# Optimization experiments

Hardware: AMD Instinct MI355X
Metric: run time of the kernel (lower is better)

The kernel has to match this reference:

```python
import jax, jax.numpy as jnp
import numpy as np

D_IN = 1024
D_OUT = 1024


def setup_inputs() -> dict:
    key = jax.random.key(0)
    k_x, k_q, k_k, k_v = jax.random.split(key, 4)
    x = jax.random.normal(k_x, (8, 2048, D_IN), dtype=jnp.float32)
    s = 1.0 / np.sqrt(D_IN)
    W_query = jax.random.uniform(k_q, (D_IN, D_OUT), jnp.float32, -s, s)
    W_key = jax.random.uniform(k_k, (D_IN, D_OUT), jnp.float32, -s, s)
    W_value = jax.random.uniform(k_v, (D_IN, D_OUT), jnp.float32, -s, s)
    return {"x": x, "W_query": W_query, "W_key": W_key, "W_value": W_value}


def reference(x, W_query, W_key, W_value):
    # x: [B, N, d_in]; weights stored as [d_in, d_out] (already transposed vs torch Linear)
    B, N, _ = x.shape
    q = x @ W_query          # [B, N, d_out]
    k = x @ W_key
    v = x @ W_value
    scores = jnp.einsum('bnd,bmd->bnm', q, k)  # [B, N, N]
    causal = jnp.tril(jnp.ones((N, N), dtype=bool))
    scores = jnp.where(causal, scores, -jnp.inf)
    weights = jax.nn.softmax(scores / np.sqrt(D_OUT), axis=-1)
    # dropout p=0.0 -> identity
    return jnp.einsum('bnm,bmd->bnd', weights, v)
```

## Files before the change

### kernel.cpp

```cpp
#include <hip/hip_runtime.h>
#include <hip/hip_bf16.h>

typedef unsigned short u16;
typedef unsigned int u32;
typedef __bf16 bf16x8 __attribute__((ext_vector_type(8)));
typedef float f32x4 __attribute__((ext_vector_type(4)));
typedef unsigned int u32x4 __attribute__((ext_vector_type(4)));

#define BATCH 8
#define SEQ   2048
#define DIM   1024
#define M_TOT (BATCH * SEQ)
#define N_QKV (3 * DIM)

#define OFF_QKV  ((size_t)0)
#define OFF_VT   ((size_t)100663296)
#define OFF_C    ((size_t)134217728)
#define OFF_XB   OFF_C
#define OFF_WT   (OFF_C + (size_t)33554432)
#define OFF_S    OFF_C

__device__ __forceinline__ u16 f32_to_bf16(float f) {
    u32 u = __builtin_bit_cast(u32, f);
    u = (u + 0x7fffu + ((u >> 16) & 1u)) >> 16;
    return (u16)u;
}

__device__ __forceinline__ float bf16_to_f32(u16 h) {
    u32 u = ((u32)h) << 16;
    return __builtin_bit_cast(float, u);
}

__device__ __forceinline__ bf16x8 lds_load8(const u16* p) {
    return __builtin_bit_cast(bf16x8, *(const u32x4*)p);
}

#define UNIT 8192

__device__ __forceinline__ void stage_unit(const u16* g, size_t lda, int k0,
                                           u16* lds, int tid) {
    int wv = tid >> 6;
#pragma unroll
    for (int iss = 0; iss < 2; ++iss) {
        int s = iss * 512 + tid;
        int row = s >> 2;
        int kg = (s & 3) ^ (row & 3);
        const u16* gp = g + (size_t)row * lda + (k0 + (kg << 3));
        u16* lp = lds + (size_t)(iss * 512 + wv * 64) * 8;
        __builtin_amdgcn_global_load_lds((const __attribute__((address_space(1))) void*)gp,
                                         (__attribute__((address_space(3))) void*)lp,
                                         16, 0, 0);
    }
}

template <int MH>
__device__ __forceinline__ void mfma_phase(const u16* uA, const u16* uB, int lane,
                                           int wm, int wn, f32x4 acc[8][4]) {
    int lrow = lane & 15;
    int off = (((lane >> 4) ^ (lane & 3)) << 3);
    bf16x8 a[4], b[4];
#pragma unroll
    for (int i = 0; i < 4; ++i) {
        a[i] = lds_load8(&uA[(wm * 128 + (MH * 4 + i) * 16 + lrow) * 32 + off]);
        b[i] = lds_load8(&uB[(wn * 64 + i * 16 + lrow) * 32 + off]);
    }
    __builtin_amdgcn_s_setprio(1);
#pragma unroll
    for (int i = 0; i < 4; ++i)
#pragma unroll
        for (int j = 0; j < 4; ++j)
            acc[MH * 4 + i][j] =
                __builtin_amdgcn_mfma_f32_16x16x32_bf16(a[i], b[j], acc[MH * 4 + i][j], 0, 0, 0);
    __builtin_amdgcn_s_setprio(0);
}

__device__ __forceinline__ void gemm_block_256(const u16* __restrict__ A, size_t lda,
                                               const u16* __restrict__ B, size_t ldb,
                                               int KT, u16* lds, int tid,
                                               f32x4 acc[8][4]) {
    int lane = tid & 63;
    int wv = tid >> 6;
    int wm = wv >> 2, wn = wv & 3;
    stage_unit(A, lda, 0,  lds + 0 * UNIT, tid);
    stage_unit(B, ldb, 0,  lds + 4 * UNIT, tid);
    stage_unit(A, lda, 32, lds + 1 * UNIT, tid);
    stage_unit(B, ldb, 32, lds + 5 * UNIT, tid);
    for (int t = 0; t < KT; ++t) {
        int p = t & 1, pn = p ^ 1;
        int kb = (t + 1) << 6;
        bool pf = (t + 1 < KT);
        asm volatile("s_waitcnt vmcnt(4)" ::: "memory");
        __builtin_amdgcn_s_barrier();
        if (pf) stage_unit(A, lda, kb, lds + (size_t)(pn * 2) * UNIT, tid);
        mfma_phase<0>(lds + (size_t)(p * 2) * UNIT, lds + (size_t)(4 + p * 2) * UNIT,
                      lane, wm, wn, acc);
        __builtin_amdgcn_s_barrier();
        if (pf) stage_unit(B, ldb, kb, lds + (size_t)(4 + pn * 2) * UNIT, tid);
        mfma_phase<1>(lds + (size_t)(p * 2) * UNIT, lds + (size_t)(4 + p * 2) * UNIT,
                      lane, wm, wn, acc);
        __builtin_amdgcn_s_barrier();
        if (pf) { asm volatile("s_waitcnt vmcnt(4)" ::: "memory"); }
        else    { asm volatile("s_waitcnt vmcnt(0)" ::: "memory"); }
        __builtin_amdgcn_s_barrier();
        if (pf) stage_unit(A, lda, kb + 32, lds + (size_t)(pn * 2 + 1) * UNIT, tid);
        mfma_phase<0>(lds + (size_t)(p * 2 + 1) * UNIT, lds + (size_t)(4 + p * 2 + 1) * UNIT,
                      lane, wm, wn, acc);
        __builtin_amdgcn_s_barrier();
        if (pf) stage_unit(B, ldb, kb + 32, lds + (size_t)(4 + pn * 2 + 1) * UNIT, tid);
        mfma_phase<1>(lds + (size_t)(p * 2 + 1) * UNIT, lds + (size_t)(4 + p * 2 + 1) * UNIT,
                      lane, wm, wn, acc);
    }
}

__global__ __launch_bounds__(256) void cast_x_kernel(const float* __restrict__ x,
                                                     u16* __restrict__ xb) {
    size_t g = (size_t)blockIdx.x * 256 + threadIdx.x;
    f32x4 v = ((const f32x4*)x)[g];
    u16 o[4] = {f32_to_bf16(v.x), f32_to_bf16(v.y), f32_to_bf16(v.z), f32_to_bf16(v.w)};
    *(unsigned long long*)(xb + g * 4) = *(const unsigned long long*)o;
}

__global__ __launch_bounds__(256) void transpose_w_kernel(const float* __restrict__ wq,
                                                          const float* __restrict__ wk,
                                                          const float* __restrict__ wv,
                                                          u16* __restrict__ wt) {
    __shared__ __align__(16) u16 tile[64][80];
    const float* w = blockIdx.z == 0 ? wq : (blockIdx.z == 1 ? wk : wv);
    int k0 = blockIdx.x * 64, n0 = blockIdx.y * 64;
    for (int g = threadIdx.x; g < 1024; g += 256) {
        int r = g >> 4, c = (g & 15) << 2;
        f32x4 v = *(const f32x4*)(w + (size_t)(k0 + r) * 1024 + n0 + c);
        tile[r][c + 0] = f32_to_bf16(v.x);
        tile[r][c + 1] = f32_to_bf16(v.y);
        tile[r][c + 2] = f32_to_bf16(v.z);
        tile[r][c + 3] = f32_to_bf16(v.w);
    }
    __syncthreads();
    u16* out = wt + (size_t)blockIdx.z * 1024 * 1024;
    for (int g = threadIdx.x; g < 512; g += 256) {
        int nr = g >> 3, kc = (g & 7) << 3;
        __align__(16) u16 tmp[8];
#pragma unroll
        for (int i = 0; i < 8; ++i) tmp[i] = tile[kc + i][nr];
        *(u32x4*)(out + (size_t)(n0 + nr) * 1024 + k0 + kc) = *(const u32x4*)tmp;
    }
}

__global__ __launch_bounds__(512, 2) void gemm_qkv_kernel(const u16* __restrict__ xb,
                                                          const u16* __restrict__ wt,
                                                          u16* __restrict__ qkv) {
    __shared__ __align__(16) u16 lds[8 * UNIT];
    int wg = blockIdx.x;
    int qx = gridDim.x >> 3;
    int swz = (wg & 7) * qx + (wg >> 3);
    int mt = swz / 12, nt = swz - mt * 12;
    const u16* A = xb + (size_t)mt * 256 * 1024;
    const u16* B = wt + (size_t)nt * 256 * 1024;
    int tid = threadIdx.x;
    f32x4 acc[8][4] = {};
    gemm_block_256(A, 1024, B, 1024, 16, lds, tid, acc);
    int lane = tid & 63, wv = tid >> 6;
    int wm = wv >> 2, wn = wv & 3;
    int r0 = (lane >> 4) << 2, c0 = lane & 15;
    size_t mbase = (size_t)mt * 256 + wm * 128;
    int nbase = nt * 256 + wn * 64;
#pragma unroll
    for (int i = 0; i < 8; ++i)
#pragma unroll
        for (int j = 0; j < 4; ++j) {
            int col = nbase + j * 16 + c0;
            float scale = (col < 1024) ? 0.03125f : 1.0f;
#pragma unroll
            for (int r = 0; r < 4; ++r) {
                size_t row = mbase + i * 16 + r0 + r;
                qkv[row * (size_t)N_QKV + col] = f32_to_bf16(acc[i][j][r] * scale);
            }
        }
}

__global__ __launch_bounds__(256) void transpose_v_kernel(const u16* __restrict__ qkv,
                                                          u16* __restrict__ vt) {
    __shared__ __align__(16) u16 tile[64][80];
    int m0 = blockIdx.x * 64, d0 = blockIdx.y * 64, b = blockIdx.z;
    const u16* src = qkv + (size_t)b * SEQ * N_QKV + 2048;
    for (int g = threadIdx.x; g < 512; g += 256) {
        int r = g >> 3, c = (g & 7) << 3;
        *(u32x4*)&tile[r][c] = *(const u32x4*)(src + (size_t)(m0 + r) * N_QKV + d0 + c);
    }
    __syncthreads();
    u16* dst = vt + (size_t)b * DIM * SEQ;
    for (int g = threadIdx.x; g < 512; g += 256) {
        int dr = g >> 3, mc = (g & 7) << 3;
        __align__(16) u16 tmp[8];
#pragma unroll
        for (int i = 0; i < 8; ++i) tmp[i] = tile[mc + i][dr];
        *(u32x4*)(dst + (size_t)(d0 + dr) * SEQ + m0 + mc) = *(const u32x4*)tmp;
    }
}

__global__ __launch_bounds__(512, 2) void gemm_scores_kernel(const u16* __restrict__ qkv,
                                                             u16* __restrict__ S) {
    __shared__ __align__(16) u16 lds[8 * UNIT];
    int t = blockIdx.x;
    int b = blockIdx.y;
    int ntile = 0;
#pragma unroll
    for (int it = 1; it < 8; ++it)
        if ((it * (it + 1)) / 2 <= t) ntile = it;
    int mtile = t - (ntile * (ntile + 1)) / 2;
    const u16* A = qkv + (size_t)b * SEQ * N_QKV + (size_t)ntile * 256 * N_QKV;
    const u16* B = qkv + (size_t)b * SEQ * N_QKV + (size_t)mtile * 256 * N_QKV + 1024;
    int tid = threadIdx.x;
    f32x4 acc[8][4] = {};
    gemm_block_256(A, N_QKV, B, N_QKV, 16, lds, tid, acc);
    u16* out = S + (size_t)b * SEQ * SEQ + (size_t)ntile * 256 * SEQ + (size_t)mtile * 256;
    int lane = tid & 63, wv = tid >> 6;
    int wm = wv >> 2, wn = wv & 3;
    int r0 = (lane >> 4) << 2, c0 = lane & 15;
#pragma unroll
    for (int i = 0; i < 8; ++i)
#pragma unroll
        for (int j = 0; j < 4; ++j) {
            int col = wn * 64 + j * 16 + c0;
#pragma unroll
            for (int r = 0; r < 4; ++r) {
                int row = wm * 128 + i * 16 + r0 + r;
                out[(size_t)row * SEQ + col] = f32_to_bf16(acc[i][j][r]);
            }
        }
}

__global__ __launch_bounds__(256) void softmax_kernel(u16* __restrict__ SP) {
    int gr = blockIdx.x;
    int n = gr & 2047;
    u16* s = SP + (size_t)gr * SEQ;
    __shared__ float red[4];
    int t = threadIdx.x;
    int base = t << 3;
    int len = n + 1;
    float v[8];
    float lmax = -3.0e38f;
    if (base < len) {
        u32x4 raw = *(const u32x4*)(s + base);
        const u16* h = (const u16*)&raw;
#pragma unroll
        for (int i = 0; i < 8; ++i) {
            v[i] = (base + i < len) ? bf16_to_f32(h[i]) : -3.0e38f;
            lmax = fmaxf(lmax, v[i]);
        }
    } else {
#pragma unroll
        for (int i = 0; i < 8; ++i) v[i] = -3.0e38f;
    }
#pragma unroll
    for (int off = 32; off; off >>= 1) lmax = fmaxf(lmax, __shfl_xor(lmax, off, 64));
    if ((t & 63) == 0) red[t >> 6] = lmax;
    __syncthreads();
    float gmax = fmaxf(fmaxf(red[0], red[1]), fmaxf(red[2], red[3]));
    __syncthreads();
    float lsum = 0.f;
#pragma unroll
    for (int i = 0; i < 8; ++i) {
        float e = __expf(v[i] - gmax);
        v[i] = e;
        lsum += e;
    }
#pragma unroll
    for (int off = 32; off; off >>= 1) lsum += __shfl_xor(lsum, off, 64);
    if ((t & 63) == 0) red[t >> 6] = lsum;
    __syncthreads();
    float inv = 1.0f / (red[0] + red[1] + red[2] + red[3]);
    __align__(16) u16 o[8];
#pragma unroll
    for (int i = 0; i < 8; ++i) o[i] = f32_to_bf16(v[i] * inv);
    *(u32x4*)(s + base) = *(const u32x4*)o;
}

__global__ __launch_bounds__(512, 2) void gemm_out_kernel(const u16* __restrict__ P,
                                                          const u16* __restrict__ vt,
                                                          float* __restrict__ O) {
    __shared__ __align__(16) u16 lds[8 * UNIT];
    int dt = blockIdx.x, b = blockIdx.z;
    int ntile = (SEQ / 256 - 1) - blockIdx.y;
    const u16* A = P + (size_t)b * SEQ * SEQ + (size_t)ntile * 256 * SEQ;
    const u16* B = vt + (size_t)b * DIM * SEQ + (size_t)dt * 256 * SEQ;
    int tid = threadIdx.x;
    f32x4 acc[8][4] = {};
    int KT = (ntile + 1) * 4;
    gemm_block_256(A, SEQ, B, SEQ, KT, lds, tid, acc);
    float* out = O + (size_t)b * SEQ * DIM + (size_t)ntile * 256 * DIM + (size_t)dt * 256;
    int lane = tid & 63, wv = tid >> 6;
    int wm = wv >> 2, wn = wv & 3;
    int r0 = (lane >> 4) << 2, c0 = lane & 15;
#pragma unroll
    for (int i = 0; i < 8; ++i)
#pragma unroll
        for (int j = 0; j < 4; ++j) {
            int col = wn * 64 + j * 16 + c0;
#pragma unroll
            for (int r = 0; r < 4; ++r) {
                int row = wm * 128 + i * 16 + r0 + r;
                out[(size_t)row * DIM + col] = acc[i][j][r];
            }
        }
}

extern "C" void kernel_launch(void* const* d_in, const int* in_sizes, int n_in,
                              void* d_out, int out_size, void* d_ws, size_t ws_size,
                              hipStream_t stream) {
    const float* x = (const float*)d_in[0];
    const float* wq = (const float*)d_in[1];
    const float* wk = (const float*)d_in[2];
    const float* wv = (const float*)d_in[3];
    char* ws = (char*)d_ws;
    u16* qkv = (u16*)(ws + OFF_QKV);
    u16* vt = (u16*)(ws + OFF_VT);
    u16* xb = (u16*)(ws + OFF_XB);
    u16* wt = (u16*)(ws + OFF_WT);
    u16* S = (u16*)(ws + OFF_S);
    float* O = (float*)d_out;

    cast_x_kernel<<<M_TOT * DIM / 4 / 256, 256, 0, stream>>>(x, xb);
    transpose_w_kernel<<<dim3(16, 16, 3), 256, 0, stream>>>(wq, wk, wv, wt);
    gemm_qkv_kernel<<<(M_TOT / 256) * (N_QKV / 256), 512, 0, stream>>>(xb, wt, qkv);
    transpose_v_kernel<<<dim3(SEQ / 64, DIM / 64, BATCH), 256, 0, stream>>>(qkv, vt);
    gemm_scores_kernel<<<dim3(36, BATCH), 512, 0, stream>>>(qkv, S);
    softmax_kernel<<<BATCH * SEQ, 256, 0, stream>>>(S);
    gemm_out_kernel<<<dim3(DIM / 256, SEQ / 256, BATCH), 512, 0, stream>>>(S, vt, O);
}
```

Before: 401.9 us.

## Deepen GEMM prefetch to a five-slot ring and remap blocks across XCDs

Result: faster. 393.3 us (-2.2%).

```diff
diff --git a/kernel.cpp b/kernel.cpp
--- a/kernel.cpp
+++ b/kernel.cpp
@@ -35,35 +35,39 @@
     return __builtin_bit_cast(bf16x8, *(const u32x4*)p);
 }
 
-#define UNIT 8192
-
-__device__ __forceinline__ void stage_unit(const u16* g, size_t lda, int k0,
-                                           u16* lds, int tid) {
+#define U4 2048
+#define NSLOT 20
+
+__device__ __forceinline__ void stage_pair(const u16* g, size_t lda, int k0,
+                                           int qbase, u16* lpair, int tid) {
     int wv = tid >> 6;
-#pragma unroll
-    for (int iss = 0; iss < 2; ++iss) {
-        int s = iss * 512 + tid;
-        int row = s >> 2;
-        int kg = (s & 3) ^ (row & 3);
-        const u16* gp = g + (size_t)row * lda + (k0 + (kg << 3));
-        u16* lp = lds + (size_t)(iss * 512 + wv * 64) * 8;
-        __builtin_amdgcn_global_load_lds((const __attribute__((address_space(1))) void*)gp,
-                                         (__attribute__((address_space(3))) void*)lp,
-                                         16, 0, 0);
+    int lane = tid & 63;
+    int u = wv >> 2;
+    int su = ((wv & 3) << 6) + lane;
+    int row = su >> 2, sc = su & 3;
+    int c = sc ^ ((row >> 1) & 3);
+    const u16* gp = g + (size_t)((qbase + u) * 64 + row) * lda + k0 + (c << 3);
+    u16* lp = lpair + u * U4 + ((wv & 3) << 9);
+    __builtin_amdgcn_global_load_lds((const __attribute__((address_space(1))) void*)gp,
+                                     (__attribute__((address_space(3))) void*)lp,
+                                     16, 0, 0);
+}
+
+template <bool LOADB>
+__device__ __forceinline__ void frags_read(const u16* uA, const u16* uB, int lane,
+                                           bf16x8 a[4], bf16x8 b[4]) {
+    int lrow = lane & 15, kgl = lane >> 4;
+    int sl = (kgl ^ ((lrow >> 1) & 3)) << 3;
+#pragma unroll
+    for (int i = 0; i < 4; ++i) {
+        a[i] = lds_load8(&uA[(i * 16 + lrow) * 32 + sl]);
+        if (LOADB) b[i] = lds_load8(&uB[(i * 16 + lrow) * 32 + sl]);
     }
 }
 
 template <int MH>
-__device__ __forceinline__ void mfma_phase(const u16* uA, const u16* uB, int lane,
-                                           int wm, int wn, f32x4 acc[8][4]) {
-    int lrow = lane & 15;
-    int off = (((lane >> 4) ^ (lane & 3)) << 3);
-    bf16x8 a[4], b[4];
-#pragma unroll
-    for (int i = 0; i < 4; ++i) {
-        a[i] = lds_load8(&uA[(wm * 128 + (MH * 4 + i) * 16 + lrow) * 32 + off]);
-        b[i] = lds_load8(&uB[(wn * 64 + i * 16 + lrow) * 32 + off]);
-    }
+__device__ __forceinline__ void mfma16(const bf16x8 a[4], const bf16x8 b[4],
+                                       f32x4 acc[8][4]) {
     __builtin_amdgcn_s_setprio(1);
 #pragma unroll
     for (int i = 0; i < 4; ++i)
@@ -76,39 +80,55 @@
 
 __device__ __forceinline__ void gemm_block_256(const u16* __restrict__ A, size_t lda,
                                                const u16* __restrict__ B, size_t ldb,
-                                               int KT, u16* lds, int tid,
+                                               int KT, u16* ldsA, u16* ldsB, int tid,
                                                f32x4 acc[8][4]) {
     int lane = tid & 63;
     int wv = tid >> 6;
     int wm = wv >> 2, wn = wv & 3;
-    stage_unit(A, lda, 0,  lds + 0 * UNIT, tid);
-    stage_unit(B, ldb, 0,  lds + 4 * UNIT, tid);
-    stage_unit(A, lda, 32, lds + 1 * UNIT, tid);
-    stage_unit(B, ldb, 32, lds + 5 * UNIT, tid);
+#pragma unroll
+    for (int pt = 0; pt < 4; ++pt) {
+        stage_pair(A, lda, pt << 5, 0, ldsA + (pt * 4 + 0) * U4, tid);
+        stage_pair(A, lda, pt << 5, 2, ldsA + (pt * 4 + 2) * U4, tid);
+        stage_pair(B, ldb, pt << 5, 0, ldsB + (pt * 4 + 0) * U4, tid);
+        stage_pair(B, ldb, pt << 5, 2, ldsB + (pt * 4 + 2) * U4, tid);
+    }
+    asm volatile("s_waitcnt vmcnt(12)" ::: "memory");
+    __builtin_amdgcn_s_barrier();
+    int rt = 0, rs = 4;
     for (int t = 0; t < KT; ++t) {
-        int p = t & 1, pn = p ^ 1;
-        int kb = (t + 1) << 6;
-        bool pf = (t + 1 < KT);
-        asm volatile("s_waitcnt vmcnt(4)" ::: "memory");
+        const u16* uA0 = ldsA + (rt * 4 + wm * 2) * U4;
+        const u16* uA1 = uA0 + U4;
+        const u16* uB  = ldsB + (rt * 4 + wn) * U4;
+        bool pf = (t + 4 < KT);
+        int k4 = (t + 4) << 5;
+        bf16x8 a[4], b[4];
+        frags_read<true>(uA0, uB, lane, a, b);
+        if (pf) {
+            stage_pair(A, lda, k4, 0, ldsA + (rs * 4 + 0) * U4, tid);
+            stage_pair(A, lda, k4, 2, ldsA + (rs * 4 + 2) * U4, tid);
+        }
         __builtin_amdgcn_s_barrier();
-        if (pf) stage_unit(A, lda, kb, lds + (size_t)(pn * 2) * UNIT, tid);
-        mfma_phase<0>(lds + (size_t)(p * 2) * UNIT, lds + (size_t)(4 + p * 2) * UNIT,
-                      lane, wm, wn, acc);
+        asm volatile("s_waitcnt lgkmcnt(0)" ::: "memory");
+        mfma16<0>(a, b, acc);
         __builtin_amdgcn_s_barrier();
-        if (pf) stage_unit(B, ldb, kb, lds + (size_t)(4 + pn * 2) * UNIT, tid);
-        mfma_phase<1>(lds + (size_t)(p * 2) * UNIT, lds + (size_t)(4 + p * 2) * UNIT,
-                      lane, wm, wn, acc);
+        frags_read<false>(uA1, uB, lane, a, b);
+        if (pf) {
+            stage_pair(B, ldb, k4, 0, ldsB + (rs * 4 + 0) * U4, tid);
+            stage_pair(B, ldb, k4, 2, ldsB + (rs * 4 + 2) * U4, tid);
+            asm volatile("s_waitcnt vmcnt(12)" ::: "memory");
+        } else if (t + 3 < KT) {
+            asm volatile("s_waitcnt vmcnt(8)" ::: "memory");
+        } else if (t + 2 < KT) {
+            asm volatile("s_waitcnt vmcnt(4)" ::: "memory");
+        } else if (t + 1 < KT) {
+            asm volatile("s_waitcnt vmcnt(0)" ::: "memory");
+        }
         __builtin_amdgcn_s_barrier();
-        if (pf) { asm volatile("s_waitcnt vmcnt(4)" ::: "memory"); }
-        else    { asm volatile("s_waitcnt vmcnt(0)" ::: "memory"); }
+        asm volatile("s_waitcnt lgkmcnt(0)" ::: "memory");
+        mfma16<1>(a, b, acc);
         __builtin_amdgcn_s_barrier();
-        if (pf) stage_unit(A, lda, kb + 32, lds + (size_t)(pn * 2 + 1) * UNIT, tid);
-        mfma_phase<0>(lds + (size_t)(p * 2 + 1) * UNIT, lds + (size_t)(4 + p * 2 + 1) * UNIT,
-                      lane, wm, wn, acc);
-        __builtin_amdgcn_s_barrier();
-        if (pf) stage_unit(B, ldb, kb + 32, lds + (size_t)(4 + pn * 2 + 1) * UNIT, tid);
-        mfma_phase<1>(lds + (size_t)(p * 2 + 1) * UNIT, lds + (size_t)(4 + p * 2 + 1) * UNIT,
-                      lane, wm, wn, acc);
+        rt = (rt == 4) ? 0 : rt + 1;
+        rs = (rs == 4) ? 0 : rs + 1;
     }
 }
 
@@ -149,16 +169,21 @@
 __global__ __launch_bounds__(512, 2) void gemm_qkv_kernel(const u16* __restrict__ xb,
                                                           const u16* __restrict__ wt,
                                                           u16* __restrict__ qkv) {
-    __shared__ __align__(16) u16 lds[8 * UNIT];
+    __shared__ __align__(16) u16 lds[2 * NSLOT * U4];
+    u16* ldsA = lds;
+    u16* ldsB = lds + NSLOT * U4;
     int wg = blockIdx.x;
-    int qx = gridDim.x >> 3;
-    int swz = (wg & 7) * qx + (wg >> 3);
-    int mt = swz / 12, nt = swz - mt * 12;
+    int xcd = wg & 7;
+    int r = wg >> 3;
+    int ng = r >> 5;
+    int j = r & 31;
+    int mt = xcd * 8 + (j & 7);
+    int nt = ng * 4 + (j >> 3);
     const u16* A = xb + (size_t)mt * 256 * 1024;
     const u16* B = wt + (size_t)nt * 256 * 1024;
     int tid = threadIdx.x;
     f32x4 acc[8][4] = {};
-    gemm_block_256(A, 1024, B, 1024, 16, lds, tid, acc);
+    gemm_block_256(A, 1024, B, 1024, 32, ldsA, ldsB, tid, acc);
     int lane = tid & 63, wv = tid >> 6;
     int wm = wv >> 2, wn = wv & 3;
     int r0 = (lane >> 4) << 2, c0 = lane & 15;
@@ -167,13 +192,13 @@
 #pragma unroll
     for (int i = 0; i < 8; ++i)
 #pragma unroll
-        for (int j = 0; j < 4; ++j) {
-            int col = nbase + j * 16 + c0;
+        for (int jj = 0; jj < 4; ++jj) {
+            int col = nbase + jj * 16 + c0;
             float scale = (col < 1024) ? 0.03125f : 1.0f;
 #pragma unroll
-            for (int r = 0; r < 4; ++r) {
-                size_t row = mbase + i * 16 + r0 + r;
-                qkv[row * (size_t)N_QKV + col] = f32_to_bf16(acc[i][j][r] * scale);
+            for (int rr = 0; rr < 4; ++rr) {
+                size_t row = mbase + i * 16 + r0 + rr;
+                qkv[row * (size_t)N_QKV + col] = f32_to_bf16(acc[i][jj][rr] * scale);
             }
         }
 }
@@ -200,9 +225,12 @@
 
 __global__ __launch_bounds__(512, 2) void gemm_scores_kernel(const u16* __restrict__ qkv,
                                                              u16* __restrict__ S) {
-    __shared__ __align__(16) u16 lds[8 * UNIT];
-    int t = blockIdx.x;
-    int b = blockIdx.y;
+    __shared__ __align__(16) u16 lds[2 * NSLOT * U4];
+    u16* ldsA = lds;
+    u16* ldsB = lds + NSLOT * U4;
+    int wg = blockIdx.x;
+    int b = wg & 7;
+    int t = wg >> 3;
     int ntile = 0;
 #pragma unroll
     for (int it = 1; it < 8; ++it)
@@ -212,7 +240,7 @@
     const u16* B = qkv + (size_t)b * SEQ * N_QKV + (size_t)mtile * 256 * N_QKV + 1024;
     int tid = threadIdx.x;
     f32x4 acc[8][4] = {};
-    gemm_block_256(A, N_QKV, B, N_QKV, 16, lds, tid, acc);
+    gemm_block_256(A, N_QKV, B, N_QKV, 32, ldsA, ldsB, tid, acc);
     u16* out = S + (size_t)b * SEQ * SEQ + (size_t)ntile * 256 * SEQ + (size_t)mtile * 256;
     int lane = tid & 63, wv = tid >> 6;
     int wm = wv >> 2, wn = wv & 3;
@@ -220,12 +248,12 @@
 #pragma unroll
     for (int i = 0; i < 8; ++i)
 #pragma unroll
-        for (int j = 0; j < 4; ++j) {
-            int col = wn * 64 + j * 16 + c0;
-#pragma unroll
-            for (int r = 0; r < 4; ++r) {
-                int row = wm * 128 + i * 16 + r0 + r;
-                out[(size_t)row * SEQ + col] = f32_to_bf16(acc[i][j][r]);
+        for (int jj = 0; jj < 4; ++jj) {
+            int col = wn * 64 + jj * 16 + c0;
+#pragma unroll
+            for (int rr = 0; rr < 4; ++rr) {
+                int row = wm * 128 + i * 16 + r0 + rr;
+                out[(size_t)row * SEQ + col] = f32_to_bf16(acc[i][jj][rr]);
             }
         }
 }
@@ -279,15 +307,20 @@
 __global__ __launch_bounds__(512, 2) void gemm_out_kernel(const u16* __restrict__ P,
                                                           const u16* __restrict__ vt,
                                                           float* __restrict__ O) {
-    __shared__ __align__(16) u16 lds[8 * UNIT];
-    int dt = blockIdx.x, b = blockIdx.z;
-    int ntile = (SEQ / 256 - 1) - blockIdx.y;
+    __shared__ __align__(16) u16 lds[2 * NSLOT * U4];
+    u16* ldsA = lds;
+    u16* ldsB = lds + NSLOT * U4;
+    int wg = blockIdx.x;
+    int b = wg & 7;
+    int r = wg >> 3;
+    int dt = r & 3;
+    int ntile = r >> 2;
     const u16* A = P + (size_t)b * SEQ * SEQ + (size_t)ntile * 256 * SEQ;
     const u16* B = vt + (size_t)b * DIM * SEQ + (size_t)dt * 256 * SEQ;
     int tid = threadIdx.x;
     f32x4 acc[8][4] = {};
-    int KT = (ntile + 1) * 4;
-    gemm_block_256(A, SEQ, B, SEQ, KT, lds, tid, acc);
+    int KT = (ntile + 1) * 8;
+    gemm_block_256(A, SEQ, B, SEQ, KT, ldsA, ldsB, tid, acc);
     float* out = O + (size_t)b * SEQ * DIM + (size_t)ntile * 256 * DIM + (size_t)dt * 256;
     int lane = tid & 63, wv = tid >> 6;
     int wm = wv >> 2, wn = wv & 3;
@@ -295,12 +328,12 @@
 #pragma unroll
     for (int i = 0; i < 8; ++i)
 #pragma unroll
-        for (int j = 0; j < 4; ++j) {
-            int col = wn * 64 + j * 16 + c0;
-#pragma unroll
-            for (int r = 0; r < 4; ++r) {
-                int row = wm * 128 + i * 16 + r0 + r;
-                out[(size_t)row * DIM + col] = acc[i][j][r];
+        for (int jj = 0; jj < 4; ++jj) {
+            int col = wn * 64 + jj * 16 + c0;
+#pragma unroll
+            for (int rr = 0; rr < 4; ++rr) {
+                int row = wm * 128 + i * 16 + r0 + rr;
+                out[(size_t)row * DIM + col] = acc[i][jj][rr];
             }
         }
 }
@@ -324,7 +357,7 @@
     transpose_w_kernel<<<dim3(16, 16, 3), 256, 0, stream>>>(wq, wk, wv, wt);
     gemm_qkv_kernel<<<(M_TOT / 256) * (N_QKV / 256), 512, 0, stream>>>(xb, wt, qkv);
     transpose_v_kernel<<<dim3(SEQ / 64, DIM / 64, BATCH), 256, 0, stream>>>(qkv, vt);
-    gemm_scores_kernel<<<dim3(36, BATCH), 512, 0, stream>>>(qkv, S);
+    gemm_scores_kernel<<<36 * BATCH, 512, 0, stream>>>(qkv, S);
     softmax_kernel<<<BATCH * SEQ, 256, 0, stream>>>(S);
-    gemm_out_kernel<<<dim3(DIM / 256, SEQ / 256, BATCH), 512, 0, stream>>>(S, vt, O);
-}
+    gemm_out_kernel<<<(DIM / 256) * (SEQ / 256) * BATCH, 512, 0, stream>>>(S, vt, O);
+}
```
